# Kernel optimization log

Hardware: AMD Instinct MI355X
Metric: run time of the kernel (lower is better)

The kernel has to match this reference:

```python
import jax, jax.numpy as jnp
import numpy as np
import math

DIM = 1024
NUM_HEADS = 16
HEAD_DIM = DIM // NUM_HEADS
LOGIT_SCALE_MAX = math.log(1.0 / 0.01)
EPS = 1e-12  # F.normalize eps


def setup_inputs() -> dict:
    key = jax.random.key(0)
    ks = jax.random.split(key, 4)
    L, N, C = 1024, 8, DIM
    scale = HEAD_DIM ** -0.5
    x = jax.random.normal(ks[0], (L, N, C), dtype=jnp.float32)
    in_proj_weight = jax.random.normal(ks[1], (3 * C, C), dtype=jnp.float32) * scale
    in_proj_bias = jnp.zeros((3 * C,), dtype=jnp.float32)
    logit_scale = jnp.full((NUM_HEADS, 1, 1), math.log(10.0), dtype=jnp.float32)
    head_scale = jnp.ones((NUM_HEADS, 1, 1), dtype=jnp.float32)
    out_w = jax.random.normal(ks[2], (C, C), dtype=jnp.float32) * (C ** -0.5)
    out_b = jax.random.normal(ks[3], (C,), dtype=jnp.float32) * 0.01
    return {"x": x, "in_proj_weight": in_proj_weight, "in_proj_bias": in_proj_bias,
            "logit_scale": logit_scale, "head_scale": head_scale,
            "out_w": out_w, "out_b": out_b}


def _l2_normalize(t):
    # matches F.normalize(t, dim=-1): t / max(||t||_2, eps)
    n = jnp.sqrt(jnp.sum(t * t, axis=-1, keepdims=True))
    return t / jnp.maximum(n, EPS)


def reference(x, in_proj_weight, in_proj_bias, logit_scale, head_scale, out_w, out_b):
    L, N, C = x.shape
    H, hd = NUM_HEADS, HEAD_DIM
    qkv = x @ in_proj_weight.T + in_proj_bias          # (L, N, 3C)
    q, k, v = jnp.split(qkv, 3, axis=-1)               # each (L, N, C)

    def to_heads(t):  # (L, N, C) -> (N, H, L, hd)
        return t.reshape(L, N, H, hd).transpose(1, 2, 0, 3)

    q, k, v = to_heads(q), to_heads(k), to_heads(v)
    # scaled-cosine attention
    ls = jnp.exp(jnp.minimum(logit_scale, LOGIT_SCALE_MAX))  # (H,1,1) broadcasts
    attn = jnp.einsum('nhld,nhmd->nhlm', _l2_normalize(q), _l2_normalize(k)) * ls
    attn = jax.nn.softmax(attn, axis=-1)               # (N, H, L, L)
    o = jnp.einsum('nhlm,nhmd->nhld', attn, v)         # (N, H, L, hd)
    o = o * head_scale                                  # per-head scale
    o = o.transpose(2, 0, 1, 3).reshape(L, N, C)       # back to (L, N, C)
    return o @ out_w.T + out_b
```

## Files before the change

### kernel.cpp

```cpp
#include <hip/hip_runtime.h>
#include <hip/hip_bf16.h>

typedef __hip_bfloat16 bf16;
typedef __attribute__((ext_vector_type(8))) short bf16x8;
typedef __attribute__((ext_vector_type(4))) float f32x4;

#define LOGIT_MAX 4.6051702f

__device__ __forceinline__ float4 load4(const float* p) { return *(const float4*)p; }

__device__ __forceinline__ void stf(float* p, float v) { *p = v; }
__device__ __forceinline__ void stf(bf16*  p, float v) { *p = __float2bfloat16(v); }

__device__ __forceinline__ void store4bf(bf16* p, float4 v) {
    union { bf16 b[4]; uint2 u; } t;
    t.b[0] = __float2bfloat16(v.x); t.b[1] = __float2bfloat16(v.y);
    t.b[2] = __float2bfloat16(v.z); t.b[3] = __float2bfloat16(v.w);
    *(uint2*)p = t.u;
}

__device__ __forceinline__ void async16(const bf16* g, const bf16* lds) {
    __builtin_amdgcn_global_load_lds(
        (const __attribute__((address_space(1))) void*)g,
        (__attribute__((address_space(3))) void*)lds, 16, 0, 0);
}

__global__ void detect_kernel(const unsigned short* __restrict__ x, int* __restrict__ flag)
{
    __shared__ int cnt;
    if (threadIdx.x == 0) cnt = 0;
    __syncthreads();
    int c = 0;
    for (int i = threadIdx.x; i < 4096; i += 256) {
        const unsigned e = (x[i] >> 7) & 0xFF;
        if (e >= 0x90) c++;
    }
    atomicAdd(&cnt, c);
    __syncthreads();
    if (threadIdx.x == 0) *flag = (cnt > 64) ? 1 : 0;
}

__global__ __launch_bounds__(256) void prep_kernel(
    const int* __restrict__ flag,
    const void* __restrict__ x, const void* __restrict__ w_in, const void* __restrict__ out_w,
    const void* __restrict__ b_in, const void* __restrict__ out_b,
    const void* __restrict__ ls, const void* __restrict__ hs,
    bf16* __restrict__ xb, bf16* __restrict__ wb, bf16* __restrict__ owb,
    float* __restrict__ smallf)
{
    const int f = *flag;
    if (blockIdx.x == 0) {
        for (int idx = threadIdx.x; idx < 4128; idx += 256) {
            float v;
            if (f) {
                if (idx < 3072)      v = ((const float*)b_in)[idx];
                else if (idx < 4096) v = ((const float*)out_b)[idx - 3072];
                else if (idx < 4112) v = expf(fminf(((const float*)ls)[idx - 4096], LOGIT_MAX));
                else                 v = ((const float*)hs)[idx - 4112];
            } else {
                if (idx < 3072)      v = __bfloat162float(((const bf16*)b_in)[idx]);
                else if (idx < 4096) v = __bfloat162float(((const bf16*)out_b)[idx - 3072]);
                else if (idx < 4112) v = expf(fminf(__bfloat162float(((const bf16*)ls)[idx - 4096]), LOGIT_MAX));
                else                 v = __bfloat162float(((const bf16*)hs)[idx - 4112]);
            }
            smallf[idx] = v;
        }
    }
    if (f != 1) return;
    const size_t NX = 8388608, NW = 3145728, NO = 1048576;
    const size_t t0   = ((size_t)blockIdx.x * 256 + threadIdx.x) * 4;
    const size_t step = (size_t)gridDim.x * 256 * 4;
    for (size_t i = t0; i < NX; i += step) store4bf(xb + i, load4((const float*)x + i));
    for (size_t i = t0; i < NW; i += step) store4bf(wb + i, load4((const float*)w_in + i));
    for (size_t i = t0; i < NO; i += step) store4bf(owb + i, load4((const float*)out_w + i));
}

__global__ __launch_bounds__(256, 3) void qkv_gemm_mfma_kernel(
    const int* __restrict__ flag,
    const bf16* __restrict__ Xws, const bf16* __restrict__ Wws,
    const bf16* __restrict__ Xdir, const bf16* __restrict__ Wdir,
    const float* __restrict__ bias_f,
    bf16* __restrict__ q, bf16* __restrict__ k, bf16* __restrict__ vt)
{
    const bf16* X = (*flag) ? Xws : Xdir;
    const bf16* W = (*flag) ? Wws : Wdir;
    __shared__ bf16 A_lds[128 * 64];
    __shared__ bf16 B_lds[128 * 64];
    const int tid  = threadIdx.x;
    const int w    = tid >> 6;
    const int lane = tid & 63;
    const int l16  = lane & 15, quad = lane >> 4;
    const int wm   = w >> 1, wn = w & 1;
    const int row0 = blockIdx.y * 128;
    const int col0 = blockIdx.x * 128;
    const int sr   = lane >> 3, sc = lane & 7;
    const int scg  = sc ^ sr;

    f32x4 acc[4][4] = {};

    for (int kt = 0; kt < 1024; kt += 64) {
        __syncthreads();
#pragma unroll
        for (int i = 0; i < 4; i++) {
            const int br = w * 32 + i * 8;
            async16(X + (size_t)(row0 + br + sr) * 1024 + kt + scg * 8, &A_lds[br * 64]);
            async16(W + (size_t)(col0 + br + sr) * 1024 + kt + scg * 8, &B_lds[br * 64]);
        }
        __syncthreads();

#pragma unroll
        for (int kh = 0; kh < 2; kh++) {
            bf16x8 af[4], bf[4];
#pragma unroll
            for (int mt = 0; mt < 4; mt++) {
                const int row = wm * 64 + mt * 16 + l16;
                af[mt] = *(const bf16x8*)&A_lds[row * 64 + (((quad + kh * 4) ^ (row & 7)) * 8)];
            }
#pragma unroll
            for (int nt = 0; nt < 4; nt++) {
                const int row = wn * 64 + nt * 16 + l16;
                bf[nt] = *(const bf16x8*)&B_lds[row * 64 + (((quad + kh * 4) ^ (row & 7)) * 8)];
            }
#pragma unroll
            for (int mt = 0; mt < 4; mt++)
#pragma unroll
                for (int nt = 0; nt < 4; nt++)
                    acc[mt][nt] = __builtin_amdgcn_mfma_f32_16x16x32_bf16(af[mt], bf[nt], acc[mt][nt], 0, 0, 0);
        }
    }

    const int cbase = col0 + wn * 64;
    const int part  = cbase >> 10;
    const int h     = (cbase & 1023) >> 6;
    float bias[4];
#pragma unroll
    for (int nt = 0; nt < 4; nt++) bias[nt] = bias_f[cbase + nt * 16 + l16];

    if (part < 2) {
        bf16* dst0 = (part == 0) ? q : k;
#pragma unroll
        for (int mt = 0; mt < 4; mt++) {
#pragma unroll
            for (int rg = 0; rg < 4; rg++) {
                const int r = row0 + wm * 64 + mt * 16 + quad * 4 + rg;
                const int l = r >> 3, nn = r & 7;
                float val[4]; float ss = 0.f;
#pragma unroll
                for (int nt = 0; nt < 4; nt++) {
                    val[nt] = acc[mt][nt][rg] + bias[nt];
                    ss += val[nt] * val[nt];
                }
                ss += __shfl_xor(ss, 1); ss += __shfl_xor(ss, 2);
                ss += __shfl_xor(ss, 4); ss += __shfl_xor(ss, 8);
                const float inv = 1.f / fmaxf(sqrtf(ss), 1e-12f);
                bf16* dp = dst0 + ((size_t)((nn * 16 + h) * 1024 + l)) * 64;
#pragma unroll
                for (int nt = 0; nt < 4; nt++)
                    dp[nt * 16 + l16] = __float2bfloat16(val[nt] * inv);
            }
        }
    } else {
#pragma unroll
        for (int mt = 0; mt < 4; mt++) {
#pragma unroll
            for (int rg = 0; rg < 4; rg++) {
                const int r = row0 + wm * 64 + mt * 16 + quad * 4 + rg;
                const int l = r >> 3, nn = r & 7;
#pragma unroll
                for (int nt = 0; nt < 4; nt++) {
                    const int d = nt * 16 + l16;
                    vt[((size_t)((nn * 16 + h) * 64 + d)) * 1024 + l] =
                        __float2bfloat16(acc[mt][nt][rg] + bias[nt]);
                }
            }
        }
    }
}

__global__ __launch_bounds__(256, 4) void attn_mfma_kernel(
    const bf16* __restrict__ q, const bf16* __restrict__ k,
    const bf16* __restrict__ vt, const float* __restrict__ scale_f,
    bf16* __restrict__ o)
{
    __shared__ bf16 K_lds[64][64];
    __shared__ bf16 Vt_lds[64][64];
    __shared__ bf16 P_lds[4][32][72];
    __shared__ float l_lds[4][32];

    const int bid  = blockIdx.x;
    const int qt   = bid >> 7;
    const int nh   = bid & 127;
    const int h    = nh & 15;
    const int n    = nh >> 4;
    const int tid  = threadIdx.x;
    const int w    = tid >> 6;
    const int lane = tid & 63;
    const int l16  = lane & 15;
    const int quad = lane >> 4;

    const size_t base = (size_t)nh * (1024 * 64);
    const float ls   = scale_f[4096 + h];
    const float hs   = scale_f[4112 + h];
    const float lsl2 = ls * 1.4426950408889634f;

    bf16x8 qf[2][2];
#pragma unroll
    for (int u = 0; u < 2; u++) {
        const int qrow = qt * 128 + w * 32 + u * 16 + l16;
        const bf16* qp = q + base + (size_t)qrow * 64 + quad * 8;
        qf[u][0] = *(const bf16x8*)qp;
        qf[u][1] = *(const bf16x8*)(qp + 32);
    }

    f32x4 o_acc[2][4] = {};
    float l_part[2] = {0.f, 0.f};

    const int sr = lane >> 3;
    const int sc = lane & 7;

    for (int j0 = 0; j0 < 1024; j0 += 64) {
        __syncthreads();
#pragma unroll
        for (int half = 0; half < 2; half++) {
            const int br  = w * 16 + half * 8;
            const int row = br + sr;
            const int cg  = sc ^ (row & 7);
            async16(k  + base + (size_t)(j0 + row) * 64 + cg * 8, &K_lds[br][0]);
            async16(vt + base + (size_t)row * 1024 + j0 + cg * 8, &Vt_lds[br][0]);
        }
        __syncthreads();

        f32x4 s8[2][4];
#pragma unroll
        for (int s = 0; s < 4; s++) {
            const int krow = s * 16 + l16;
            const int swz  = krow & 7;
            const bf16x8 kf0 = *(const bf16x8*)&K_lds[krow][(quad ^ swz) * 8];
            const bf16x8 kf1 = *(const bf16x8*)&K_lds[krow][((quad + 4) ^ swz) * 8];
#pragma unroll
            for (int u = 0; u < 2; u++) {
                f32x4 a = {};
                a = __builtin_amdgcn_mfma_f32_16x16x32_bf16(kf0, qf[u][0], a, 0, 0, 0);
                a = __builtin_amdgcn_mfma_f32_16x16x32_bf16(kf1, qf[u][1], a, 0, 0, 0);
                s8[u][s] = a;
            }
        }

#pragma unroll
        for (int u = 0; u < 2; u++) {
#pragma unroll
            for (int s = 0; s < 4; s++) {
                union { bf16 b[4]; uint2 uu; } pk;
                float sum = 0.f;
#pragma unroll
                for (int r = 0; r < 4; r++) {
                    const float p = exp2f(fmaf(s8[u][s][r], lsl2, -lsl2));
                    pk.b[r] = __float2bfloat16(p);
                    sum += p;
                }
                l_part[u] += sum;
                *(uint2*)&P_lds[w][u * 16 + l16][s * 16 + quad * 4] = pk.uu;
            }
        }

        bf16x8 pf[2][2];
#pragma unroll
        for (int u = 0; u < 2; u++) {
            pf[u][0] = *(const bf16x8*)&P_lds[w][u * 16 + l16][quad * 8];
            pf[u][1] = *(const bf16x8*)&P_lds[w][u * 16 + l16][32 + quad * 8];
        }
#pragma unroll
        for (int ds = 0; ds < 4; ds++) {
            const int vrow = ds * 16 + l16;
            const int swz  = vrow & 7;
            const bf16x8 vf0 = *(const bf16x8*)&Vt_lds[vrow][(quad ^ swz) * 8];
            const bf16x8 vf1 = *(const bf16x8*)&Vt_lds[vrow][((quad + 4) ^ swz) * 8];
#pragma unroll
            for (int u = 0; u < 2; u++) {
                o_acc[u][ds] = __builtin_amdgcn_mfma_f32_16x16x32_bf16(pf[u][0], vf0, o_acc[u][ds], 0, 0, 0);
                o_acc[u][ds] = __builtin_amdgcn_mfma_f32_16x16x32_bf16(pf[u][1], vf1, o_acc[u][ds], 0, 0, 0);
            }
        }
    }

#pragma unroll
    for (int u = 0; u < 2; u++) {
        float v = l_part[u];
        v += __shfl_xor(v, 16);
        v += __shfl_xor(v, 32);
        l_lds[w][u * 16 + l16] = v;
    }

#pragma unroll
    for (int u = 0; u < 2; u++) {
#pragma unroll
        for (int r = 0; r < 4; r++) {
            const float inv = hs / l_lds[w][u * 16 + quad * 4 + r];
            const int row_l = qt * 128 + w * 32 + u * 16 + quad * 4 + r;
            bf16* dst = o + ((size_t)row_l * 8 + n) * 1024 + h * 64 + l16;
#pragma unroll
            for (int ds = 0; ds < 4; ds++)
                dst[ds * 16] = __float2bfloat16(o_acc[u][ds][r] * inv);
        }
    }
}

__global__ __launch_bounds__(256, 3) void out_gemm_mfma_kernel(
    const int* __restrict__ flag,
    const bf16* __restrict__ A,
    const bf16* __restrict__ Bws, const bf16* __restrict__ Bdir,
    const float* __restrict__ bias_f,
    float* __restrict__ outf, bf16* __restrict__ outb)
{
    const int f = *flag;
    const bf16* B = f ? Bws : Bdir;
    __shared__ bf16 A_lds[128 * 64];
    __shared__ bf16 B_lds[128 * 64];
    const int tid  = threadIdx.x;
    const int w    = tid >> 6;
    const int lane = tid & 63;
    const int l16  = lane & 15, quad = lane >> 4;
    const int wm   = w >> 1, wn = w & 1;
    const int row0 = blockIdx.y * 128;
    const int col0 = blockIdx.x * 128;
    const int sr   = lane >> 3, sc = lane & 7;
    const int scg  = sc ^ sr;

    f32x4 acc[4][4] = {};

    for (int kt = 0; kt < 1024; kt += 64) {
        __syncthreads();
#pragma unroll
        for (int i = 0; i < 4; i++) {
            const int br = w * 32 + i * 8;
            async16(A + (size_t)(row0 + br + sr) * 1024 + kt + scg * 8, &A_lds[br * 64]);
            async16(B + (size_t)(col0 + br + sr) * 1024 + kt + scg * 8, &B_lds[br * 64]);
        }
        __syncthreads();

#pragma unroll
        for (int kh = 0; kh < 2; kh++) {
            bf16x8 af[4], bf[4];
#pragma unroll
            for (int mt = 0; mt < 4; mt++) {
                const int row = wm * 64 + mt * 16 + l16;
                af[mt] = *(const bf16x8*)&A_lds[row * 64 + (((quad + kh * 4) ^ (row & 7)) * 8)];
            }
#pragma unroll
            for (int nt = 0; nt < 4; nt++) {
                const int row = wn * 64 + nt * 16 + l16;
                bf[nt] = *(const bf16x8*)&B_lds[row * 64 + (((quad + kh * 4) ^ (row & 7)) * 8)];
            }
#pragma unroll
            for (int mt = 0; mt < 4; mt++)
#pragma unroll
                for (int nt = 0; nt < 4; nt++)
                    acc[mt][nt] = __builtin_amdgcn_mfma_f32_16x16x32_bf16(af[mt], bf[nt], acc[mt][nt], 0, 0, 0);
        }
    }

#pragma unroll
    for (int mt = 0; mt < 4; mt++) {
        const int rbase = row0 + wm * 64 + mt * 16 + quad * 4;
#pragma unroll
        for (int nt = 0; nt < 4; nt++) {
            const int c = col0 + wn * 64 + nt * 16 + l16;
            const float bias = bias_f[c];
#pragma unroll
            for (int rg = 0; rg < 4; rg++) {
                const float v = acc[mt][nt][rg] + bias;
                const size_t idx = (size_t)(rbase + rg) * 1024 + c;
                if (f) outf[idx] = v; else outb[idx] = __float2bfloat16(v);
            }
        }
    }
}

extern "C" void kernel_launch(void* const* d_in, const int* in_sizes, int n_in,
                              void* d_out, int out_size, void* d_ws, size_t ws_size,
                              hipStream_t stream)
{
    const size_t SEG = (size_t)8 * 16 * 1024 * 64;
    bf16* qn  = (bf16*)d_ws;
    bf16* kn  = qn + SEG;
    bf16* vt  = kn + SEG;
    bf16* ow  = vt + SEG;
    bf16* xb  = ow + SEG;
    bf16* wb  = xb + SEG;
    bf16* owb = wb + 3145728;
    float* smallf = (float*)(owb + 1048576);
    int*   flag   = (int*)(smallf + 4128);

    detect_kernel<<<1, 256, 0, stream>>>((const unsigned short*)d_in[0], flag);

    prep_kernel<<<4096, 256, 0, stream>>>(flag,
        d_in[0], d_in[1], d_in[5], d_in[2], d_in[6], d_in[3], d_in[4],
        xb, wb, owb, smallf);

    qkv_gemm_mfma_kernel<<<dim3(3072 / 128, 8192 / 128), 256, 0, stream>>>(
        flag, xb, wb, (const bf16*)d_in[0], (const bf16*)d_in[1], smallf, qn, kn, vt);

    attn_mfma_kernel<<<dim3(128 * 8), 256, 0, stream>>>(qn, kn, vt, smallf, ow);

    out_gemm_mfma_kernel<<<dim3(1024 / 128, 8192 / 128), 256, 0, stream>>>(
        flag, ow, owb, (const bf16*)d_in[5], smallf + 3072,
        (float*)d_out, (bf16*)d_out);
}
```

Measured before the change: 273.4 us.

## Double-buffer GEMM mainloop with 128x256 tiles, 8 waves, and XCD-aware block mapping

```diff
diff --git a/kernel.cpp b/kernel.cpp
--- a/kernel.cpp
+++ b/kernel.cpp
@@ -8,9 +8,6 @@
 #define LOGIT_MAX 4.6051702f
 
 __device__ __forceinline__ float4 load4(const float* p) { return *(const float4*)p; }
-
-__device__ __forceinline__ void stf(float* p, float v) { *p = v; }
-__device__ __forceinline__ void stf(bf16*  p, float v) { *p = __float2bfloat16(v); }
 
 __device__ __forceinline__ void store4bf(bf16* p, float4 v) {
     union { bf16 b[4]; uint2 u; } t;
@@ -24,6 +21,13 @@
         (const __attribute__((address_space(1))) void*)g,
         (__attribute__((address_space(3))) void*)lds, 16, 0, 0);
 }
+
+__device__ __forceinline__ void wg_barrier() {
+    asm volatile("" ::: "memory");
+    __builtin_amdgcn_s_barrier();
+    asm volatile("" ::: "memory");
+}
+#define VMCNT(n) asm volatile("s_waitcnt vmcnt(" #n ")" ::: "memory")
 
 __global__ void detect_kernel(const unsigned short* __restrict__ x, int* __restrict__ flag)
 {
@@ -75,7 +79,74 @@
     for (size_t i = t0; i < NO; i += step) store4bf(owb + i, load4((const float*)out_w + i));
 }
 
-__global__ __launch_bounds__(256, 3) void qkv_gemm_mfma_kernel(
+__device__ __forceinline__ void mfma_mainloop_128x256(
+    const bf16* __restrict__ A, const bf16* __restrict__ B,
+    int row0, int col0, bf16* Ab, bf16* Bb, f32x4 (&acc)[4][4])
+{
+    const int tid  = threadIdx.x;
+    const int w    = tid >> 6;
+    const int lane = tid & 63;
+    const int l16  = lane & 15, quad = lane >> 4;
+    const int wr   = w >> 2, wc = w & 3;
+    const int srow   = tid >> 2;
+    const int schunk = (((tid & 3) ^ ((tid >> 3) & 3)) << 3);
+    const bf16* Asrc  = A + (size_t)(row0 + srow) * 1024 + schunk;
+    const bf16* Bsrc0 = B + (size_t)(col0 + srow) * 1024 + schunk;
+    const bf16* Bsrc1 = B + (size_t)(col0 + 128 + srow) * 1024 + schunk;
+    bf16* AW = Ab + w * 512;
+    bf16* BW = Bb + w * 512;
+
+#define STAGE(bufv, khv, kc) do {                                          \
+    const int _o = (kc) + (khv) * 32;                                      \
+    async16(Asrc  + _o, AW + ((bufv) * 2 + (khv)) * 4096);                 \
+    async16(Bsrc0 + _o, BW + ((bufv) * 2 + (khv)) * 8192);                 \
+    async16(Bsrc1 + _o, BW + ((bufv) * 2 + (khv)) * 8192 + 4096);          \
+} while (0)
+
+#define COMPUTE(bufv, khv) do {                                            \
+    const bf16* Ap = Ab + ((bufv) * 2 + (khv)) * 4096;                     \
+    const bf16* Bp = Bb + ((bufv) * 2 + (khv)) * 8192;                     \
+    bf16x8 af[4], bfr[4];                                                  \
+    _Pragma("unroll")                                                      \
+    for (int mt = 0; mt < 4; mt++) {                                       \
+        const int r = wr * 64 + mt * 16 + l16;                             \
+        af[mt] = *(const bf16x8*)&Ap[r * 32 + ((quad ^ ((r >> 1) & 3)) << 3)]; \
+    }                                                                      \
+    _Pragma("unroll")                                                      \
+    for (int nt = 0; nt < 4; nt++) {                                       \
+        const int r = wc * 64 + nt * 16 + l16;                             \
+        bfr[nt] = *(const bf16x8*)&Bp[r * 32 + ((quad ^ ((r >> 1) & 3)) << 3)]; \
+    }                                                                      \
+    __builtin_amdgcn_s_setprio(1);                                         \
+    _Pragma("unroll")                                                      \
+    for (int mt = 0; mt < 4; mt++)                                         \
+        _Pragma("unroll")                                                  \
+        for (int nt = 0; nt < 4; nt++)                                     \
+            acc[mt][nt] = __builtin_amdgcn_mfma_f32_16x16x32_bf16(af[mt], bfr[nt], acc[mt][nt], 0, 0, 0); \
+    __builtin_amdgcn_s_setprio(0);                                         \
+} while (0)
+
+    STAGE(0, 0, 0);
+    STAGE(0, 1, 0);
+#pragma unroll 1
+    for (int t = 0; t < 15; ++t) {
+        const int c = t & 1;
+        STAGE(c ^ 1, 0, (t + 1) * 64);
+        VMCNT(6); wg_barrier();
+        COMPUTE(c, 0);
+        STAGE(c ^ 1, 1, (t + 1) * 64);
+        VMCNT(6); wg_barrier();
+        COMPUTE(c, 1);
+    }
+    VMCNT(3); wg_barrier();
+    COMPUTE(1, 0);
+    VMCNT(0); wg_barrier();
+    COMPUTE(1, 1);
+#undef STAGE
+#undef COMPUTE
+}
+
+__global__ __launch_bounds__(512, 2) void qkv_gemm_mfma_kernel(
     const int* __restrict__ flag,
     const bf16* __restrict__ Xws, const bf16* __restrict__ Wws,
     const bf16* __restrict__ Xdir, const bf16* __restrict__ Wdir,
@@ -84,52 +155,25 @@
 {
     const bf16* X = (*flag) ? Xws : Xdir;
     const bf16* W = (*flag) ? Wws : Wdir;
-    __shared__ bf16 A_lds[128 * 64];
-    __shared__ bf16 B_lds[128 * 64];
+    __shared__ bf16 Ab[2 * 2 * 4096];
+    __shared__ bf16 Bb[2 * 2 * 8192];
+
+    const int bid = blockIdx.x;
+    const int wg  = (bid & 7) * 96 + (bid >> 3);
+    const int bx  = wg % 12, by = wg / 12;
+    const int row0 = by * 128;
+    const int col0 = bx * 256;
+
+    f32x4 acc[4][4] = {};
+    mfma_mainloop_128x256(X, W, row0, col0, Ab, Bb, acc);
+
     const int tid  = threadIdx.x;
     const int w    = tid >> 6;
     const int lane = tid & 63;
     const int l16  = lane & 15, quad = lane >> 4;
-    const int wm   = w >> 1, wn = w & 1;
-    const int row0 = blockIdx.y * 128;
-    const int col0 = blockIdx.x * 128;
-    const int sr   = lane >> 3, sc = lane & 7;
-    const int scg  = sc ^ sr;
-
-    f32x4 acc[4][4] = {};
-
-    for (int kt = 0; kt < 1024; kt += 64) {
-        __syncthreads();
-#pragma unroll
-        for (int i = 0; i < 4; i++) {
-            const int br = w * 32 + i * 8;
-            async16(X + (size_t)(row0 + br + sr) * 1024 + kt + scg * 8, &A_lds[br * 64]);
-            async16(W + (size_t)(col0 + br + sr) * 1024 + kt + scg * 8, &B_lds[br * 64]);
-        }
-        __syncthreads();
-
-#pragma unroll
-        for (int kh = 0; kh < 2; kh++) {
-            bf16x8 af[4], bf[4];
-#pragma unroll
-            for (int mt = 0; mt < 4; mt++) {
-                const int row = wm * 64 + mt * 16 + l16;
-                af[mt] = *(const bf16x8*)&A_lds[row * 64 + (((quad + kh * 4) ^ (row & 7)) * 8)];
-            }
-#pragma unroll
-            for (int nt = 0; nt < 4; nt++) {
-                const int row = wn * 64 + nt * 16 + l16;
-                bf[nt] = *(const bf16x8*)&B_lds[row * 64 + (((quad + kh * 4) ^ (row & 7)) * 8)];
-            }
-#pragma unroll
-            for (int mt = 0; mt < 4; mt++)
-#pragma unroll
-                for (int nt = 0; nt < 4; nt++)
-                    acc[mt][nt] = __builtin_amdgcn_mfma_f32_16x16x32_bf16(af[mt], bf[nt], acc[mt][nt], 0, 0, 0);
-        }
-    }
-
-    const int cbase = col0 + wn * 64;
+    const int wr   = w >> 2, wc = w & 3;
+
+    const int cbase = col0 + wc * 64;
     const int part  = cbase >> 10;
     const int h     = (cbase & 1023) >> 6;
     float bias[4];
@@ -142,7 +186,7 @@
         for (int mt = 0; mt < 4; mt++) {
 #pragma unroll
             for (int rg = 0; rg < 4; rg++) {
-                const int r = row0 + wm * 64 + mt * 16 + quad * 4 + rg;
+                const int r = row0 + wr * 64 + mt * 16 + quad * 4 + rg;
                 const int l = r >> 3, nn = r & 7;
                 float val[4]; float ss = 0.f;
 #pragma unroll
@@ -164,7 +208,7 @@
         for (int mt = 0; mt < 4; mt++) {
 #pragma unroll
             for (int rg = 0; rg < 4; rg++) {
-                const int r = row0 + wm * 64 + mt * 16 + quad * 4 + rg;
+                const int r = row0 + wr * 64 + mt * 16 + quad * 4 + rg;
                 const int l = r >> 3, nn = r & 7;
 #pragma unroll
                 for (int nt = 0; nt < 4; nt++) {
@@ -305,7 +349,7 @@
     }
 }
 
-__global__ __launch_bounds__(256, 3) void out_gemm_mfma_kernel(
+__global__ __launch_bounds__(512, 2) void out_gemm_mfma_kernel(
     const int* __restrict__ flag,
     const bf16* __restrict__ A,
     const bf16* __restrict__ Bws, const bf16* __restrict__ Bdir,
@@ -314,57 +358,30 @@
 {
     const int f = *flag;
     const bf16* B = f ? Bws : Bdir;
-    __shared__ bf16 A_lds[128 * 64];
-    __shared__ bf16 B_lds[128 * 64];
+    __shared__ bf16 Ab[2 * 2 * 4096];
+    __shared__ bf16 Bb[2 * 2 * 8192];
+
+    const int bid = blockIdx.x;
+    const int wg  = (bid & 7) * 32 + (bid >> 3);
+    const int bx  = wg & 3, by = wg >> 2;
+    const int row0 = by * 128;
+    const int col0 = bx * 256;
+
+    f32x4 acc[4][4] = {};
+    mfma_mainloop_128x256(A, B, row0, col0, Ab, Bb, acc);
+
     const int tid  = threadIdx.x;
     const int w    = tid >> 6;
     const int lane = tid & 63;
     const int l16  = lane & 15, quad = lane >> 4;
-    const int wm   = w >> 1, wn = w & 1;
-    const int row0 = blockIdx.y * 128;
-    const int col0 = blockIdx.x * 128;
-    const int sr   = lane >> 3, sc = lane & 7;
-    const int scg  = sc ^ sr;
-
-    f32x4 acc[4][4] = {};
-
-    for (int kt = 0; kt < 1024; kt += 64) {
-        __syncthreads();
-#pragma unroll
-        for (int i = 0; i < 4; i++) {
-            const int br = w * 32 + i * 8;
-            async16(A + (size_t)(row0 + br + sr) * 1024 + kt + scg * 8, &A_lds[br * 64]);
-            async16(B + (size_t)(col0 + br + sr) * 1024 + kt + scg * 8, &B_lds[br * 64]);
-        }
-        __syncthreads();
-
-#pragma unroll
-        for (int kh = 0; kh < 2; kh++) {
-            bf16x8 af[4], bf[4];
-#pragma unroll
-            for (int mt = 0; mt < 4; mt++) {
-                const int row = wm * 64 + mt * 16 + l16;
-                af[mt] = *(const bf16x8*)&A_lds[row * 64 + (((quad + kh * 4) ^ (row & 7)) * 8)];
-            }
-#pragma unroll
-            for (int nt = 0; nt < 4; nt++) {
-                const int row = wn * 64 + nt * 16 + l16;
-                bf[nt] = *(const bf16x8*)&B_lds[row * 64 + (((quad + kh * 4) ^ (row & 7)) * 8)];
-            }
-#pragma unroll
-            for (int mt = 0; mt < 4; mt++)
-#pragma unroll
-                for (int nt = 0; nt < 4; nt++)
-                    acc[mt][nt] = __builtin_amdgcn_mfma_f32_16x16x32_bf16(af[mt], bf[nt], acc[mt][nt], 0, 0, 0);
-        }
-    }
+    const int wr   = w >> 2, wc = w & 3;
 
 #pragma unroll
     for (int mt = 0; mt < 4; mt++) {
-        const int rbase = row0 + wm * 64 + mt * 16 + quad * 4;
+        const int rbase = row0 + wr * 64 + mt * 16 + quad * 4;
 #pragma unroll
         for (int nt = 0; nt < 4; nt++) {
-            const int c = col0 + wn * 64 + nt * 16 + l16;
+            const int c = col0 + wc * 64 + nt * 16 + l16;
             const float bias = bias_f[c];
 #pragma unroll
             for (int rg = 0; rg < 4; rg++) {
@@ -397,12 +414,12 @@
         d_in[0], d_in[1], d_in[5], d_in[2], d_in[6], d_in[3], d_in[4],
         xb, wb, owb, smallf);
 
-    qkv_gemm_mfma_kernel<<<dim3(3072 / 128, 8192 / 128), 256, 0, stream>>>(
+    qkv_gemm_mfma_kernel<<<dim3(768), 512, 0, stream>>>(
         flag, xb, wb, (const bf16*)d_in[0], (const bf16*)d_in[1], smallf, qn, kn, vt);
 
     attn_mfma_kernel<<<dim3(128 * 8), 256, 0, stream>>>(qn, kn, vt, smallf, ow);
 
-    out_gemm_mfma_kernel<<<dim3(1024 / 128, 8192 / 128), 256, 0, stream>>>(
+    out_gemm_mfma_kernel<<<dim3(256), 512, 0, stream>>>(
         flag, ow, owb, (const bf16*)d_in[5], smallf + 3072,
         (float*)d_out, (bf16*)d_out);
 }
```

Measured after the change: 297.4 us. +8.8%, slower.
